# Kernel tuning notes

Measured on AMD Instinct MI355X. Metric: run time of the kernel, lower is better.

## Reference

```python
import jax, jax.numpy as jnp
import numpy as np

jax.config.update("jax_enable_x64", True)  # original casts to double for covpool/SVD

BN_EPS = 1e-5


def setup_inputs() -> dict:
    key = jax.random.key(0)
    k1, k2 = jax.random.split(key)
    x = jax.random.normal(k1, (64, 2048, 14, 14), dtype=jnp.float32)
    conv_w = jax.random.normal(k2, (256, 2048), dtype=jnp.float32) * 0.02  # 1x1 conv kernel
    bn_gamma = jnp.ones((256,), dtype=jnp.float32)
    bn_beta = jnp.zeros((256,), dtype=jnp.float32)
    return {"x": x, "conv_w": conv_w, "bn_gamma": bn_gamma, "bn_beta": bn_beta}


def reference(x, conv_w, bn_gamma, bn_beta):
    # --- dimension reduction block: 1x1 conv (no bias) + BN (train mode) + ReLU ---
    y = jnp.einsum('oc,bchw->bohw', conv_w, x)  # [B,256,14,14]
    mean = y.mean(axis=(0, 2, 3), keepdims=True)
    var = y.var(axis=(0, 2, 3), keepdims=True)
    y = (y - mean) * jax.lax.rsqrt(var + BN_EPS)
    y = y * bn_gamma[None, :, None, None] + bn_beta[None, :, None, None]
    y = jnp.maximum(y, 0.0)

    # --- Covpool: x @ (I/M - 11^T/M^2) @ x^T, in float64 as original ---
    B, d, h, w = y.shape
    M = h * w
    z = y.reshape(B, d, M).astype(jnp.float64)
    zc = z - z.mean(axis=2, keepdims=True)          # centering == multiplying by I_hat
    cov = jnp.einsum('bim,bjm->bij', zc, zc) / M    # [B,d,d], symmetric PSD

    # --- Eigen decomposition (SVD of symmetric PSD == eigh), clamp tiny eigvals ---
    s, V = jnp.linalg.eigh(cov)                     # s: [B,d], V: [B,d,d]
    eps = jnp.finfo(jnp.float64).eps
    s = jnp.maximum(s, eps)

    # --- Power: matrix square root Q = V sqrt(S) V^T ---
    Q = jnp.einsum('bij,bj,bkj->bik', V, jnp.sqrt(s), V)  # [B,d,d]

    # --- upper-triangular (incl. diag) vectorization, row-major like torch triu ---
    iu = jnp.triu_indices(d)
    q_triv = Q[:, iu[0], iu[1]]                     # [B, d*(d+1)/2]
    return q_triv.astype(jnp.float32)
```

## Files before the change

kernel.cpp:

```cpp
#include <hip/hip_runtime.h>
#include <hip/hip_bf16.h>

static constexpr int B   = 64;
static constexpr int CIN = 2048;
static constexpr int O   = 256;
static constexpr int HW  = 196;
static constexpr int D   = 256;
static constexpr int TRI = 32896;
static constexpr int NQ_COUPLED = 5;
static constexpr size_t NELEM = (size_t)B * D * D;
static constexpr size_t YN    = (size_t)B * O * HW;

typedef unsigned short u16;
typedef unsigned short u16x4 __attribute__((ext_vector_type(4)));
typedef unsigned short u16x8 __attribute__((ext_vector_type(8)));
typedef __bf16         bf16x8 __attribute__((ext_vector_type(8)));
typedef float          f32x4 __attribute__((ext_vector_type(4)));

static __device__ __forceinline__ u16 f2bf(float x) {
    unsigned int u = __float_as_uint(x);
    u += 0x7FFFu + ((u >> 16) & 1u);
    return (u16)(u >> 16);
}
static __device__ __forceinline__ float bf2f(u16 h) {
    return __uint_as_float(((unsigned int)h) << 16);
}
static __device__ __forceinline__ f32x4 mm_bf16(u16x8 a, u16x8 b, f32x4 c) {
    return __builtin_amdgcn_mfma_f32_16x16x32_bf16(
        __builtin_bit_cast(bf16x8, a), __builtin_bit_cast(bf16x8, b), c, 0, 0, 0);
}

__global__ __launch_bounds__(256) void k_wsplit(const float* __restrict__ W,
                                                u16* __restrict__ Wh,
                                                u16* __restrict__ Wl) {
    const size_t i = (size_t)blockIdx.x * 256 + threadIdx.x;
    const float v = W[i];
    const u16 h = f2bf(v);
    Wh[i] = h;
    Wl[i] = f2bf(v - bf2f(h));
}

__global__ __launch_bounds__(256, 3) void k_conv(const float* __restrict__ x,
                                                 const u16* __restrict__ Wh,
                                                 const u16* __restrict__ Wl,
                                                 float* __restrict__ psum) {
    const int l   = blockIdx.x;
    const int xcd = l & 7, u = l >> 3;
    const int q   = xcd * 98 + u;
    const int ks  = q & 3;
    const int t2  = q >> 2;
    const int ot  = t2 & 1, gt = t2 >> 1;
    const int o0  = ot * 128;
    const int cbase = ks * 512;
    float* yp = psum + (size_t)ks * YN;

    const int tid = threadIdx.x;

    __shared__ u16 sW[2][128][40], sX[2][128][40];

    const int colX  = tid & 127;
    const int chalf = (tid >> 7) * 16;
    const int gX = gt * 128 + colX;
    const int bX = gX / 196;
    const int mX = gX - bX * 196;
    const size_t xbase = (size_t)bX * (CIN * HW) + mX;

    const int rW = tid >> 1, kq = (tid & 1) * 16;
    const u16* gWh = Wh + (size_t)(o0 + rW) * CIN + cbase + kq;
    const u16* gWl = Wl + (size_t)(o0 + rW) * CIN + cbase + kq;

    const int lane = tid & 63, w = tid >> 6;
    const int wr = w >> 1, wc = w & 1;
    const int lr = lane & 15, lg = lane >> 4, ko = lg << 3;

    f32x4 acc[4][4] = {};

    u16x8 pWh[2], pWl[2];
    float pX[16];
    u16x4 cXh[4], cXl[4];

    auto loadW = [&](int kb) {
        #pragma unroll
        for (int qq = 0; qq < 2; ++qq) {
            pWh[qq] = *(const u16x8*)&gWh[kb + qq * 8];
            pWl[qq] = *(const u16x8*)&gWl[kb + qq * 8];
        }
    };
    auto loadX = [&](int kb) {
        #pragma unroll
        for (int i = 0; i < 16; ++i)
            pX[i] = x[xbase + (size_t)(cbase + kb + chalf + i) * HW];
    };
    auto convX = [&]() {
        #pragma unroll
        for (int i = 0; i < 16; i += 4) {
            u16x4 vh, vl;
            #pragma unroll
            for (int j = 0; j < 4; ++j) {
                const float v = pX[i + j];
                const u16 h = f2bf(v);
                vh[j] = h;
                vl[j] = f2bf(v - bf2f(h));
            }
            cXh[i >> 2] = vh;
            cXl[i >> 2] = vl;
        }
    };
    auto storeWX = [&]() {
        #pragma unroll
        for (int qq = 0; qq < 2; ++qq) {
            *(u16x8*)&sW[0][rW][kq + qq * 8] = pWh[qq];
            *(u16x8*)&sW[1][rW][kq + qq * 8] = pWl[qq];
        }
        #pragma unroll
        for (int qq = 0; qq < 4; ++qq) {
            *(u16x4*)&sX[0][colX][chalf + qq * 4] = cXh[qq];
            *(u16x4*)&sX[1][colX][chalf + qq * 4] = cXl[qq];
        }
    };
    auto compute = [&]() {
        u16x8 fah[4], fal[4], fbh[4], fbl[4];
        #pragma unroll
        for (int f = 0; f < 4; ++f) {
            fah[f] = *(const u16x8*)&sW[0][wr * 64 + f * 16 + lr][ko];
            fal[f] = *(const u16x8*)&sW[1][wr * 64 + f * 16 + lr][ko];
            fbh[f] = *(const u16x8*)&sX[0][wc * 64 + f * 16 + lr][ko];
            fbl[f] = *(const u16x8*)&sX[1][wc * 64 + f * 16 + lr][ko];
        }
        #pragma unroll
        for (int fi = 0; fi < 4; ++fi)
            #pragma unroll
            for (int fj = 0; fj < 4; ++fj) {
                acc[fi][fj] = mm_bf16(fah[fi], fbh[fj], acc[fi][fj]);
                acc[fi][fj] = mm_bf16(fah[fi], fbl[fj], acc[fi][fj]);
                acc[fi][fj] = mm_bf16(fal[fi], fbh[fj], acc[fi][fj]);
            }
    };

    loadW(0); loadX(0); convX();
    for (int st = 0; st < 16; ++st) {
        __syncthreads();
        storeWX();
        __syncthreads();
        if (st < 15) { loadW((st + 1) * 32); loadX((st + 1) * 32); }
        compute();
        if (st < 15) convX();
    }

    #pragma unroll
    for (int fj = 0; fj < 4; ++fj) {
        const int gcol = gt * 128 + wc * 64 + fj * 16 + lr;
        const int bb = gcol / 196;
        const int mm = gcol - bb * 196;
        const size_t ybase = (size_t)bb * (O * HW) + mm;
        #pragma unroll
        for (int fi = 0; fi < 4; ++fi)
            #pragma unroll
            for (int r = 0; r < 4; ++r) {
                const int orow = o0 + wr * 64 + fi * 16 + (lg << 2) + r;
                yp[ybase + (size_t)orow * HW] = acc[fi][fj][r];
            }
    }
}

__global__ __launch_bounds__(256) void k_redy(const float* __restrict__ ps,
                                              float* __restrict__ y) {
    const size_t i = ((size_t)blockIdx.x * 256 + threadIdx.x) * 4;
    if (i >= YN) return;
    float4 a = *(const float4*)&ps[i];
    const float4 b = *(const float4*)&ps[YN + i];
    const float4 c = *(const float4*)&ps[2 * YN + i];
    const float4 d = *(const float4*)&ps[3 * YN + i];
    a.x += b.x + c.x + d.x; a.y += b.y + c.y + d.y;
    a.z += b.z + c.z + d.z; a.w += b.w + c.w + d.w;
    *(float4*)&y[i] = a;
}

__global__ __launch_bounds__(256) void k_bnstats(const float* __restrict__ y,
                                                 const float* __restrict__ gamma,
                                                 const float* __restrict__ beta,
                                                 float* __restrict__ scl,
                                                 float* __restrict__ shf) {
    const int o = blockIdx.x;
    const int tid = threadIdx.x;
    float s = 0.f, s2 = 0.f;
    if (tid < HW) {
        for (int b = 0; b < B; ++b) {
            const float v = y[((size_t)b * O + o) * HW + tid];
            s += v; s2 += v * v;
        }
    }
    #pragma unroll
    for (int msk = 32; msk; msk >>= 1) {
        s  += __shfl_xor(s,  msk);
        s2 += __shfl_xor(s2, msk);
    }
    __shared__ float rs[4], rs2[4];
    if ((tid & 63) == 0) { rs[tid >> 6] = s; rs2[tid >> 6] = s2; }
    __syncthreads();
    if (tid == 0) {
        const float N = (float)(B * HW);
        const float ts  = rs[0] + rs[1] + rs[2] + rs[3];
        const float ts2 = rs2[0] + rs2[1] + rs2[2] + rs2[3];
        const float mean = ts / N;
        const float var  = ts2 / N - mean * mean;
        const float sc = gamma[o] * rsqrtf(var + 1e-5f);
        scl[o] = sc;
        shf[o] = beta[o] - mean * sc;
    }
}

__global__ __launch_bounds__(64) void k_center(float* __restrict__ z,
                                               const float* __restrict__ scl,
                                               const float* __restrict__ shf) {
    const int row = blockIdx.x;
    const int o = row & 255;
    const int lane = threadIdx.x;
    const float sc = scl[o], sh = shf[o];
    float* zr = &z[(size_t)row * HW];
    float vals[4];
    float s = 0.f;
    #pragma unroll
    for (int q = 0; q < 4; ++q) {
        const int m = q * 64 + lane;
        float v = 0.f;
        if (m < HW) v = fmaxf(fmaf(zr[m], sc, sh), 0.f);
        vals[q] = v; s += v;
    }
    #pragma unroll
    for (int msk = 32; msk; msk >>= 1) s += __shfl_xor(s, msk);
    const float mean = s / (float)HW;
    #pragma unroll
    for (int q = 0; q < 4; ++q) {
        const int m = q * 64 + lane;
        if (m < HW) zr[m] = vals[q] - mean;
    }
}

__global__ __launch_bounds__(256) void k_cov(const float* __restrict__ z,
                                             float* __restrict__ covf) {
    const int b = blockIdx.y;
    const int jt = blockIdx.x & 3, it = blockIdx.x >> 2;
    const int i0 = it * 64, j0 = jt * 64;
    const int tid = threadIdx.x;
    const int tn = tid & 15, tmq = tid >> 4;

    __shared__ float sA[28][68], sB[28][68];
    double acc[4][4] = {};
    const float* zb = &z[(size_t)b * D * HW];

    for (int k0 = 0; k0 < HW; k0 += 28) {
        #pragma unroll
        for (int q = 0; q < 7; ++q) {
            const int idx = tid + q * 256;
            const int r = idx / 28, kk = idx % 28;
            sA[kk][r] = zb[(size_t)(i0 + r) * HW + k0 + kk];
            sB[kk][r] = zb[(size_t)(j0 + r) * HW + k0 + kk];
        }
        __syncthreads();
        #pragma unroll
        for (int kk = 0; kk < 28; ++kk) {
            const float4 av = *reinterpret_cast<const float4*>(&sA[kk][tmq << 2]);
            const float4 bv = *reinterpret_cast<const float4*>(&sB[kk][tn << 2]);
            const double aa[4] = {av.x, av.y, av.z, av.w};
            const double bb[4] = {bv.x, bv.y, bv.z, bv.w};
            #pragma unroll
            for (int i = 0; i < 4; ++i)
                #pragma unroll
                for (int j = 0; j < 4; ++j)
                    acc[i][j] = fma(aa[i], bb[j], acc[i][j]);
        }
        __syncthreads();
    }
    const double inv = 1.0 / (double)HW;
    #pragma unroll
    for (int i = 0; i < 4; ++i)
        #pragma unroll
        for (int j = 0; j < 4; ++j)
            covf[(size_t)b * D * D + (size_t)(i0 + (tmq << 2) + i) * D
                 + j0 + (tn << 2) + j] = (float)(acc[i][j] * inv);
}

__global__ __launch_bounds__(256) void k_lmax(const float* __restrict__ covf,
                                              double* __restrict__ cn) {
    const int b = blockIdx.x;
    const int tid = threadIdx.x;
    const float* A = &covf[(size_t)b * 65536];
    __shared__ float vs[256];
    __shared__ float red[4];
    vs[tid] = 1.f;
    __syncthreads();
    float lam = 1.f;
    for (int it = 0; it < 6; ++it) {
        float u0 = 0.f, u1 = 0.f, u2 = 0.f, u3 = 0.f;
        #pragma unroll 8
        for (int k = 0; k < D; k += 4) {
            u0 = fmaf(A[(size_t)(k + 0) * D + tid], vs[k + 0], u0);
            u1 = fmaf(A[(size_t)(k + 1) * D + tid], vs[k + 1], u1);
            u2 = fmaf(A[(size_t)(k + 2) * D + tid], vs[k + 2], u2);
            u3 = fmaf(A[(size_t)(k + 3) * D + tid], vs[k + 3], u3);
        }
        const float uu = (u0 + u1) + (u2 + u3);
        float sq = uu * uu;
        #pragma unroll
        for (int msk = 32; msk; msk >>= 1) sq += __shfl_xor(sq, msk);
        __syncthreads();
        if ((tid & 63) == 0) red[tid >> 6] = sq;
        __syncthreads();
        const float nrm = sqrtf(red[0] + red[1] + red[2] + red[3]) + 1e-30f;
        lam = nrm;
        vs[tid] = uu / nrm;
        __syncthreads();
    }
    if (tid == 0) cn[b] = (lam > 1e-30f) ? 1.25 * (double)lam : 1.0;
}

__global__ __launch_bounds__(256) void k_init(const float* __restrict__ covf,
                                              const double* __restrict__ cn,
                                              u16* __restrict__ Yh,
                                              u16* __restrict__ Yl) {
    const size_t e = (size_t)blockIdx.x * 256 + threadIdx.x;
    const int b = (int)(e >> 16);
    const int ij = (int)(e & 65535);
    const float diag = ((ij >> 8) == (ij & 255)) ? 1e-7f : 0.f;
    const float f = covf[e] / (float)cn[b] + diag;
    const u16 h = f2bf(f);
    Yh[e] = h;
    Yl[e] = f2bf(f - bf2f(h));
}

template <int MODE, int FUSED>
__global__ __launch_bounds__(256, 2) void k_mgemm(
        const u16* __restrict__ A0h, const u16* __restrict__ A0l,
        const u16* __restrict__ B0h, const u16* __restrict__ B0l,
        u16* __restrict__ C0h, u16* __restrict__ C0l,
        const u16* __restrict__ A1h, const u16* __restrict__ A1l,
        const u16* __restrict__ B1h, const u16* __restrict__ B1l,
        u16* __restrict__ C1h, u16* __restrict__ C1l,
        const double* __restrict__ cn, float* __restrict__ outp) {
    const int orig = blockIdx.x;
    const int xcd  = orig & 7;
    const int s    = orig >> 3;
    int batch, task, opz;
    if (FUSED) {
        const int bl  = s / 12;
        const int rem = s - bl * 12;
        opz  = rem >= 6;
        task = rem - opz * 6;
        batch = xcd * 8 + bl;
    } else {
        opz = 0;
        const int bl = s / 6;
        task = s - bl * 6;
        batch = xcd * 8 + bl;
    }

    const u16 *Ah, *Al, *Bh, *Bl;
    u16 *Ch, *Cl;
    if (opz == 0) { Ah = A0h; Al = A0l; Bh = B0h; Bl = B0l; Ch = C0h; Cl = C0l; }
    else          { Ah = A1h; Al = A1l; Bh = B1h; Bl = B1l; Ch = C1h; Cl = C1l; }

    const int it = task >> 2;
    const int jt = (task < 4) ? task : task - 2;
    const int i0 = it * 128, j0 = jt * 64;
    const size_t boff = (size_t)batch * 65536;
    Ah += boff; Al += boff; Bh += boff; Bl += boff; Ch += boff; Cl += boff;

    const int tid = threadIdx.x;
    __shared__ u16 sA[2][128][72];
    __shared__ u16 sB[2][64][72];

    const int rA = tid >> 1, khA = (tid & 1) * 32;
    const u16* gAh = Ah + (size_t)(i0 + rA) * 256 + khA;
    const u16* gAl = Al + (size_t)(i0 + rA) * 256 + khA;
    const int rB = tid >> 2, khB = (tid & 3) * 16;
    const u16* gBh = Bh + (size_t)(j0 + rB) * 256 + khB;
    const u16* gBl = Bl + (size_t)(j0 + rB) * 256 + khB;

    const int lane = tid & 63, w = tid >> 6;
    const int wr = w >> 1, wc = w & 1;
    const int lr = lane & 15, lg = lane >> 4, ko = lg << 3;

    f32x4 acc[4][2] = {};

    u16x8 pAh[4], pAl[4], pBh[2], pBl[2];
    auto g_load = [&](int kb) {
        #pragma unroll
        for (int qq = 0; qq < 4; ++qq) {
            pAh[qq] = *(const u16x8*)&gAh[kb + qq * 8];
            pAl[qq] = *(const u16x8*)&gAl[kb + qq * 8];
        }
        #pragma unroll
        for (int qq = 0; qq < 2; ++qq) {
            pBh[qq] = *(const u16x8*)&gBh[kb + qq * 8];
            pBl[qq] = *(const u16x8*)&gBl[kb + qq * 8];
        }
    };
    auto s_store = [&]() {
        #pragma unroll
        for (int qq = 0; qq < 4; ++qq) {
            *(u16x8*)&sA[0][rA][khA + qq * 8] = pAh[qq];
            *(u16x8*)&sA[1][rA][khA + qq * 8] = pAl[qq];
        }
        #pragma unroll
        for (int qq = 0; qq < 2; ++qq) {
            *(u16x8*)&sB[0][rB][khB + qq * 8] = pBh[qq];
            *(u16x8*)&sB[1][rB][khB + qq * 8] = pBl[qq];
        }
    };
    auto compute = [&]() {
        #pragma unroll
        for (int kr = 0; kr < 2; ++kr) {
            const int kk = kr * 32 + ko;
            u16x8 fah[4], fal[4], fbh[2], fbl[2];
            #pragma unroll
            for (int f = 0; f < 4; ++f) {
                fah[f] = *(const u16x8*)&sA[0][wr * 64 + f * 16 + lr][kk];
                fal[f] = *(const u16x8*)&sA[1][wr * 64 + f * 16 + lr][kk];
            }
            #pragma unroll
            for (int f = 0; f < 2; ++f) {
                fbh[f] = *(const u16x8*)&sB[0][wc * 32 + f * 16 + lr][kk];
                fbl[f] = *(const u16x8*)&sB[1][wc * 32 + f * 16 + lr][kk];
            }
            #pragma unroll
            for (int fi = 0; fi < 4; ++fi)
                #pragma unroll
                for (int fj = 0; fj < 2; ++fj) {
                    acc[fi][fj] = mm_bf16(fah[fi], fbh[fj], acc[fi][fj]);
                    acc[fi][fj] = mm_bf16(fah[fi], fbl[fj], acc[fi][fj]);
                    acc[fi][fj] = mm_bf16(fal[fi], fbh[fj], acc[fi][fj]);
                }
        }
    };

    g_load(0);
    for (int st = 0; st < 4; ++st) {
        __syncthreads();
        s_store();
        __syncthreads();
        if (st < 3) g_load((st + 1) * 64);
        compute();
    }

    const int orow = wr * 64 + (lg << 2);
    const int ocol = wc * 32 + lr;

    if (MODE == 3) {
        const double sc = sqrt(cn[batch]);
        #pragma unroll
        for (int fi = 0; fi < 4; ++fi)
            #pragma unroll
            for (int r = 0; r < 4; ++r) {
                const int gi = i0 + orow + fi * 16 + r;
                const size_t rowoff = (size_t)gi * D - ((size_t)gi * (gi - 1)) / 2;
                #pragma unroll
                for (int fj = 0; fj < 2; ++fj) {
                    const int gj = j0 + ocol + fj * 16;
                    if (gj >= gi)
                        outp[(size_t)batch * TRI + rowoff + (gj - gi)] =
                            (float)(sc * (double)acc[fi][fj][r]);
                }
            }
        return;
    }

    u16 hv[4][4][2], lv[4][4][2];
    #pragma unroll
    for (int fi = 0; fi < 4; ++fi)
        #pragma unroll
        for (int r = 0; r < 4; ++r) {
            const int gi = i0 + orow + fi * 16 + r;
            #pragma unroll
            for (int fj = 0; fj < 2; ++fj) {
                const int gj = j0 + ocol + fj * 16;
                float v = acc[fi][fj][r];
                if (MODE == 1) {
                    const size_t xo = (size_t)gi * 256 + gj;
                    const float xv = bf2f(Ah[xo]) + bf2f(Al[xo]);
                    v = (((gi == gj) ? 15.0f : 0.0f) - 10.0f * xv + 3.0f * v) * 0.125f;
                }
                const u16 h = f2bf(v);
                const u16 lo = f2bf(v - bf2f(h));
                const size_t co = (size_t)gi * 256 + gj;
                Ch[co] = h;
                Cl[co] = lo;
                hv[fi][r][fj] = h;
                lv[fi][r][fj] = lo;
            }
        }

    if (task == 2 || task == 3) {
        __syncthreads();
        u16 (*tH)[136] = reinterpret_cast<u16(*)[136]>(&sA[0][0][0]);
        u16 (*tL)[136] = reinterpret_cast<u16(*)[136]>(&sB[0][0][0]);
        #pragma unroll
        for (int fi = 0; fi < 4; ++fi)
            #pragma unroll
            for (int r = 0; r < 4; ++r) {
                const int li = orow + fi * 16 + r;
                #pragma unroll
                for (int fj = 0; fj < 2; ++fj) {
                    const int lj = ocol + fj * 16;
                    tH[lj][li] = hv[fi][r][fj];
                    tL[lj][li] = lv[fi][r][fj];
                }
            }
        __syncthreads();
        const int r2 = tid >> 2, c2 = (tid & 3) << 5;
        const size_t mo = (size_t)(j0 + r2) * 256 + i0 + c2;
        #pragma unroll
        for (int qq = 0; qq < 4; ++qq) {
            *(u16x8*)&Ch[mo + qq * 8] = *(const u16x8*)&tH[r2][c2 + qq * 8];
            *(u16x8*)&Cl[mo + qq * 8] = *(const u16x8*)&tL[r2][c2 + qq * 8];
        }
    }
}

extern "C" void kernel_launch(void* const* d_in, const int* in_sizes, int n_in,
                              void* d_out, int out_size, void* d_ws, size_t ws_size,
                              hipStream_t stream) {
    const float* x     = (const float*)d_in[0];
    const float* W     = (const float*)d_in[1];
    const float* gamma = (const float*)d_in[2];
    const float* beta  = (const float*)d_in[3];
    float* out = (float*)d_out;

    char* ws = (char*)d_ws;
    size_t off = 0;
    auto alloc = [&](size_t bytes) -> void* {
        void* p = ws + off;
        off += (bytes + 255) & ~(size_t)255;
        return p;
    };
    float*  y    = (float*)alloc(YN * sizeof(float));
    float*  covf = (float*)alloc(NELEM * sizeof(float));
    float*  scl  = (float*)alloc(O * sizeof(float));
    float*  shf  = (float*)alloc(O * sizeof(float));
    double* cn   = (double*)alloc(B * sizeof(double));
    u16*    Wh   = (u16*)alloc((size_t)O * CIN * sizeof(u16));
    u16*    Wl   = (u16*)alloc((size_t)O * CIN * sizeof(u16));
    u16* pl = (u16*)alloc(12 * NELEM * sizeof(u16));
    if (off > ws_size) return;
    u16 *YAh = pl,             *YAl = pl + NELEM;
    u16 *YBh = pl + 2 * NELEM, *YBl = pl + 3 * NELEM;
    u16 *MAh = pl + 4 * NELEM, *MAl = pl + 5 * NELEM;
    u16 *MBh = pl + 6 * NELEM, *MBl = pl + 7 * NELEM;
    u16 *Rh  = pl + 8 * NELEM, *Rl  = pl + 9 * NELEM;
    u16 *Uh  = pl + 10 * NELEM,*Ul  = pl + 11 * NELEM;
    float* psum = (float*)pl;

    k_wsplit <<<(O * CIN) / 256, 256, 0, stream>>>(W, Wh, Wl);
    k_conv   <<<784, 256, 0, stream>>>(x, Wh, Wl, psum);
    k_redy   <<<3136, 256, 0, stream>>>(psum, y);
    k_bnstats<<<O, 256, 0, stream>>>(y, gamma, beta, scl, shf);
    k_center <<<B * O, 64, 0, stream>>>(y, scl, shf);
    k_cov    <<<dim3(16, B), 256, 0, stream>>>(y, covf);
    k_lmax   <<<B, 256, 0, stream>>>(covf, cn);
    k_init   <<<B * 256, 256, 0, stream>>>(covf, cn, YAh, YAl);

    k_mgemm<1, 0><<<384, 256, 0, stream>>>(YAh, YAl, YAh, YAl, Rh, Rl,
                                           YAh, YAl, YAh, YAl, Rh, Rl, cn, out);
    k_mgemm<2, 0><<<384, 256, 0, stream>>>(YAh, YAl, Rh, Rl, YBh, YBl,
                                           YAh, YAl, Rh, Rl, YBh, YBl, cn, out);
    k_mgemm<2, 0><<<384, 256, 0, stream>>>(Rh, Rl, YBh, YBl, MBh, MBl,
                                           Rh, Rl, YBh, YBl, MBh, MBl, cn, out);

    u16 *Ych = YBh, *Ycl = YBl, *Yah = YAh, *Yal = YAl;
    u16 *Mch = MBh, *Mcl = MBl, *Mah = MAh, *Mal = MAl;
    for (int itq = 0; itq < NQ_COUPLED; ++itq) {
        k_mgemm<1, 0><<<384, 256, 0, stream>>>(Mch, Mcl, Mch, Mcl, Rh, Rl,
                                               Mch, Mcl, Mch, Mcl, Rh, Rl, cn, out);
        k_mgemm<2, 1><<<768, 256, 0, stream>>>(Ych, Ycl, Rh, Rl, Yah, Yal,
                                               Mch, Mcl, Rh, Rl, Uh, Ul, cn, out);
        k_mgemm<2, 0><<<384, 256, 0, stream>>>(Rh, Rl, Uh, Ul, Mah, Mal,
                                               Rh, Rl, Uh, Ul, Mah, Mal, cn, out);
        u16* t;
        t = Ych; Ych = Yah; Yah = t;  t = Ycl; Ycl = Yal; Yal = t;
        t = Mch; Mch = Mah; Mah = t;  t = Mcl; Mcl = Mal; Mal = t;
    }
    k_mgemm<1, 0><<<384, 256, 0, stream>>>(Mch, Mcl, Mch, Mcl, Rh, Rl,
                                           Mch, Mcl, Mch, Mcl, Rh, Rl, cn, out);
    k_mgemm<3, 0><<<384, 256, 0, stream>>>(Ych, Ycl, Rh, Rl, Uh, Ul,
                                           Ych, Ycl, Rh, Rl, Uh, Ul, cn, out);
}
```

Baseline: 508.3 us.

## Compute full matrix tiles with smaller k-step and fuse partial-sum reduction into BN stats

The matrix-iteration GEMM stops exploiting symmetry: it now computes all 8 output tiles per batch instead of 6 plus a transpose write. It shrinks the shared-memory k-step from 64 to 32 so that 3 blocks fit per CU, and stages the epilogue through LDS for coalesced vector stores and vectorized loads of the residual operand. Separately, the split-K partial-sum reduction kernel is folded into the BN statistics kernel, removing one launch and one pass over y. This adds a third more MFMA work per GEMM in exchange for higher occupancy, uniform tiles and coalesced epilogues.

Measured after the change: 576.1 us. 1.13x slower.

```diff
diff --git a/kernel.cpp b/kernel.cpp
--- a/kernel.cpp
+++ b/kernel.cpp
@@ -163,20 +163,8 @@
     }
 }
 
-__global__ __launch_bounds__(256) void k_redy(const float* __restrict__ ps,
-                                              float* __restrict__ y) {
-    const size_t i = ((size_t)blockIdx.x * 256 + threadIdx.x) * 4;
-    if (i >= YN) return;
-    float4 a = *(const float4*)&ps[i];
-    const float4 b = *(const float4*)&ps[YN + i];
-    const float4 c = *(const float4*)&ps[2 * YN + i];
-    const float4 d = *(const float4*)&ps[3 * YN + i];
-    a.x += b.x + c.x + d.x; a.y += b.y + c.y + d.y;
-    a.z += b.z + c.z + d.z; a.w += b.w + c.w + d.w;
-    *(float4*)&y[i] = a;
-}
-
-__global__ __launch_bounds__(256) void k_bnstats(const float* __restrict__ y,
+__global__ __launch_bounds__(256) void k_bnstats(const float* __restrict__ ps,
+                                                 float* __restrict__ y,
                                                  const float* __restrict__ gamma,
                                                  const float* __restrict__ beta,
                                                  float* __restrict__ scl,
@@ -186,7 +174,10 @@
     float s = 0.f, s2 = 0.f;
     if (tid < HW) {
         for (int b = 0; b < B; ++b) {
-            const float v = y[((size_t)b * O + o) * HW + tid];
+            const size_t idx = ((size_t)b * O + o) * HW + tid;
+            const float v = ps[idx] + ps[YN + idx] + ps[2 * YN + idx]
+                          + ps[3 * YN + idx];
+            y[idx] = v;
             s += v; s2 += v * v;
         }
     }
@@ -330,7 +321,7 @@
 }
 
 template <int MODE, int FUSED>
-__global__ __launch_bounds__(256, 2) void k_mgemm(
+__global__ __launch_bounds__(256, 3) void k_mgemm(
         const u16* __restrict__ A0h, const u16* __restrict__ A0l,
         const u16* __restrict__ B0h, const u16* __restrict__ B0l,
         u16* __restrict__ C0h, u16* __restrict__ C0l,
@@ -341,18 +332,17 @@
     const int orig = blockIdx.x;
     const int xcd  = orig & 7;
     const int s    = orig >> 3;
-    int batch, task, opz;
+    int batch, tile, opz;
     if (FUSED) {
-        const int bl  = s / 12;
-        const int rem = s - bl * 12;
-        opz  = rem >= 6;
-        task = rem - opz * 6;
+        const int bl  = s >> 4;
+        const int opq = s & 15;
+        opz  = opq >> 3;
+        tile = opq & 7;
         batch = xcd * 8 + bl;
     } else {
         opz = 0;
-        const int bl = s / 6;
-        task = s - bl * 6;
-        batch = xcd * 8 + bl;
+        batch = xcd * 8 + (s >> 3);
+        tile = s & 7;
     }
 
     const u16 *Ah, *Al, *Bh, *Bl;
@@ -360,20 +350,23 @@
     if (opz == 0) { Ah = A0h; Al = A0l; Bh = B0h; Bl = B0l; Ch = C0h; Cl = C0l; }
     else          { Ah = A1h; Al = A1l; Bh = B1h; Bl = B1l; Ch = C1h; Cl = C1l; }
 
-    const int it = task >> 2;
-    const int jt = (task < 4) ? task : task - 2;
-    const int i0 = it * 128, j0 = jt * 64;
+    const int i0 = (tile >> 2) * 128, j0 = (tile & 3) * 64;
     const size_t boff = (size_t)batch * 65536;
     Ah += boff; Al += boff; Bh += boff; Bl += boff; Ch += boff; Cl += boff;
 
     const int tid = threadIdx.x;
-    __shared__ u16 sA[2][128][72];
-    __shared__ u16 sB[2][64][72];
-
-    const int rA = tid >> 1, khA = (tid & 1) * 32;
+    __shared__ u16 smem[18432];
+    u16* sA0 = smem;
+    u16* sA1 = smem + 5120;
+    u16* sB0 = smem + 10240;
+    u16* sB1 = smem + 12800;
+    u16* ep0 = smem;
+    u16* ep1 = smem + 9216;
+
+    const int rA = tid >> 1, khA = (tid & 1) * 16;
     const u16* gAh = Ah + (size_t)(i0 + rA) * 256 + khA;
     const u16* gAl = Al + (size_t)(i0 + rA) * 256 + khA;
-    const int rB = tid >> 2, khB = (tid & 3) * 16;
+    const int rB = tid >> 2, khB = (tid & 3) * 8;
     const u16* gBh = Bh + (size_t)(j0 + rB) * 256 + khB;
     const u16* gBl = Bl + (size_t)(j0 + rB) * 256 + khB;
 
@@ -383,63 +376,51 @@
 
     f32x4 acc[4][2] = {};
 
-    u16x8 pAh[4], pAl[4], pBh[2], pBl[2];
+    u16x8 pAh[2], pAl[2], pBh, pBl;
     auto g_load = [&](int kb) {
-        #pragma unroll
-        for (int qq = 0; qq < 4; ++qq) {
-            pAh[qq] = *(const u16x8*)&gAh[kb + qq * 8];
-            pAl[qq] = *(const u16x8*)&gAl[kb + qq * 8];
-        }
-        #pragma unroll
-        for (int qq = 0; qq < 2; ++qq) {
-            pBh[qq] = *(const u16x8*)&gBh[kb + qq * 8];
-            pBl[qq] = *(const u16x8*)&gBl[kb + qq * 8];
-        }
+        pAh[0] = *(const u16x8*)&gAh[kb];
+        pAh[1] = *(const u16x8*)&gAh[kb + 8];
+        pAl[0] = *(const u16x8*)&gAl[kb];
+        pAl[1] = *(const u16x8*)&gAl[kb + 8];
+        pBh = *(const u16x8*)&gBh[kb];
+        pBl = *(const u16x8*)&gBl[kb];
     };
     auto s_store = [&]() {
-        #pragma unroll
-        for (int qq = 0; qq < 4; ++qq) {
-            *(u16x8*)&sA[0][rA][khA + qq * 8] = pAh[qq];
-            *(u16x8*)&sA[1][rA][khA + qq * 8] = pAl[qq];
-        }
-        #pragma unroll
-        for (int qq = 0; qq < 2; ++qq) {
-            *(u16x8*)&sB[0][rB][khB + qq * 8] = pBh[qq];
-            *(u16x8*)&sB[1][rB][khB + qq * 8] = pBl[qq];
-        }
+        *(u16x8*)&sA0[rA * 40 + khA]     = pAh[0];
+        *(u16x8*)&sA0[rA * 40 + khA + 8] = pAh[1];
+        *(u16x8*)&sA1[rA * 40 + khA]     = pAl[0];
+        *(u16x8*)&sA1[rA * 40 + khA + 8] = pAl[1];
+        *(u16x8*)&sB0[rB * 40 + khB]     = pBh;
+        *(u16x8*)&sB1[rB * 40 + khB]     = pBl;
     };
     auto compute = [&]() {
-        #pragma unroll
-        for (int kr = 0; kr < 2; ++kr) {
-            const int kk = kr * 32 + ko;
-            u16x8 fah[4], fal[4], fbh[2], fbl[2];
-            #pragma unroll
-            for (int f = 0; f < 4; ++f) {
-                fah[f] = *(const u16x8*)&sA[0][wr * 64 + f * 16 + lr][kk];
-                fal[f] = *(const u16x8*)&sA[1][wr * 64 + f * 16 + lr][kk];
+        u16x8 fah[4], fal[4], fbh[2], fbl[2];
+        #pragma unroll
+        for (int f = 0; f < 4; ++f) {
+            fah[f] = *(const u16x8*)&sA0[(wr * 64 + f * 16 + lr) * 40 + ko];
+            fal[f] = *(const u16x8*)&sA1[(wr * 64 + f * 16 + lr) * 40 + ko];
+        }
+        #pragma unroll
+        for (int f = 0; f < 2; ++f) {
+            fbh[f] = *(const u16x8*)&sB0[(wc * 32 + f * 16 + lr) * 40 + ko];
+            fbl[f] = *(const u16x8*)&sB1[(wc * 32 + f * 16 + lr) * 40 + ko];
+        }
+        #pragma unroll
+        for (int fi = 0; fi < 4; ++fi)
+            #pragma unroll
+            for (int fj = 0; fj < 2; ++fj) {
+                acc[fi][fj] = mm_bf16(fah[fi], fbh[fj], acc[fi][fj]);
+                acc[fi][fj] = mm_bf16(fah[fi], fbl[fj], acc[fi][fj]);
+                acc[fi][fj] = mm_bf16(fal[fi], fbh[fj], acc[fi][fj]);
             }
-            #pragma unroll
-            for (int f = 0; f < 2; ++f) {
-                fbh[f] = *(const u16x8*)&sB[0][wc * 32 + f * 16 + lr][kk];
-                fbl[f] = *(const u16x8*)&sB[1][wc * 32 + f * 16 + lr][kk];
-            }
-            #pragma unroll
-            for (int fi = 0; fi < 4; ++fi)
-                #pragma unroll
-                for (int fj = 0; fj < 2; ++fj) {
-                    acc[fi][fj] = mm_bf16(fah[fi], fbh[fj], acc[fi][fj]);
-                    acc[fi][fj] = mm_bf16(fah[fi], fbl[fj], acc[fi][fj]);
-                    acc[fi][fj] = mm_bf16(fal[fi], fbh[fj], acc[fi][fj]);
-                }
-        }
     };
 
     g_load(0);
-    for (int st = 0; st < 4; ++st) {
+    for (int st = 0; st < 8; ++st) {
         __syncthreads();
         s_store();
         __syncthreads();
-        if (st < 3) g_load((st + 1) * 64);
+        if (st < 7) g_load((st + 1) * 32);
         compute();
     }
 
@@ -465,55 +446,49 @@
         return;
     }
 
-    u16 hv[4][4][2], lv[4][4][2];
+    __syncthreads();
+    const int er = tid >> 1, ec = (tid & 1) * 32;
+    if (MODE == 1) {
+        u16x8 th[4], tl[4];
+        #pragma unroll
+        for (int qq = 0; qq < 4; ++qq) {
+            th[qq] = *(const u16x8*)&Ah[(size_t)(i0 + er) * 256 + j0 + ec + qq * 8];
+            tl[qq] = *(const u16x8*)&Al[(size_t)(i0 + er) * 256 + j0 + ec + qq * 8];
+        }
+        #pragma unroll
+        for (int qq = 0; qq < 4; ++qq) {
+            *(u16x8*)&ep0[er * 72 + ec + qq * 8] = th[qq];
+            *(u16x8*)&ep1[er * 72 + ec + qq * 8] = tl[qq];
+        }
+        __syncthreads();
+    }
     #pragma unroll
     for (int fi = 0; fi < 4; ++fi)
         #pragma unroll
         for (int r = 0; r < 4; ++r) {
-            const int gi = i0 + orow + fi * 16 + r;
+            const int li = orow + fi * 16 + r;
             #pragma unroll
             for (int fj = 0; fj < 2; ++fj) {
-                const int gj = j0 + ocol + fj * 16;
+                const int lj = ocol + fj * 16;
                 float v = acc[fi][fj][r];
                 if (MODE == 1) {
-                    const size_t xo = (size_t)gi * 256 + gj;
-                    const float xv = bf2f(Ah[xo]) + bf2f(Al[xo]);
-                    v = (((gi == gj) ? 15.0f : 0.0f) - 10.0f * xv + 3.0f * v) * 0.125f;
+                    const float xv = bf2f(ep0[li * 72 + lj]) + bf2f(ep1[li * 72 + lj]);
+                    v = ((((i0 + li) == (j0 + lj)) ? 15.0f : 0.0f)
+                         - 10.0f * xv + 3.0f * v) * 0.125f;
                 }
                 const u16 h = f2bf(v);
                 const u16 lo = f2bf(v - bf2f(h));
-                const size_t co = (size_t)gi * 256 + gj;
-                Ch[co] = h;
-                Cl[co] = lo;
-                hv[fi][r][fj] = h;
-                lv[fi][r][fj] = lo;
+                ep0[li * 72 + lj] = h;
+                ep1[li * 72 + lj] = lo;
             }
         }
-
-    if (task == 2 || task == 3) {
-        __syncthreads();
-        u16 (*tH)[136] = reinterpret_cast<u16(*)[136]>(&sA[0][0][0]);
-        u16 (*tL)[136] = reinterpret_cast<u16(*)[136]>(&sB[0][0][0]);
-        #pragma unroll
-        for (int fi = 0; fi < 4; ++fi)
-            #pragma unroll
-            for (int r = 0; r < 4; ++r) {
-                const int li = orow + fi * 16 + r;
-                #pragma unroll
-                for (int fj = 0; fj < 2; ++fj) {
-                    const int lj = ocol + fj * 16;
-                    tH[lj][li] = hv[fi][r][fj];
-                    tL[lj][li] = lv[fi][r][fj];
-                }
-            }
-        __syncthreads();
-        const int r2 = tid >> 2, c2 = (tid & 3) << 5;
-        const size_t mo = (size_t)(j0 + r2) * 256 + i0 + c2;
-        #pragma unroll
-        for (int qq = 0; qq < 4; ++qq) {
-            *(u16x8*)&Ch[mo + qq * 8] = *(const u16x8*)&tH[r2][c2 + qq * 8];
-            *(u16x8*)&Cl[mo + qq * 8] = *(const u16x8*)&tL[r2][c2 + qq * 8];
-        }
+    __syncthreads();
+    #pragma unroll
+    for (int qq = 0; qq < 4; ++qq) {
+        *(u16x8*)&Ch[(size_t)(i0 + er) * 256 + j0 + ec + qq * 8] =
+            *(const u16x8*)&ep0[er * 72 + ec + qq * 8];
+        *(u16x8*)&Cl[(size_t)(i0 + er) * 256 + j0 + ec + qq * 8] =
+            *(const u16x8*)&ep1[er * 72 + ec + qq * 8];
     }
 }
 
@@ -552,35 +527,34 @@
 
     k_wsplit <<<(O * CIN) / 256, 256, 0, stream>>>(W, Wh, Wl);
     k_conv   <<<784, 256, 0, stream>>>(x, Wh, Wl, psum);
-    k_redy   <<<3136, 256, 0, stream>>>(psum, y);
-    k_bnstats<<<O, 256, 0, stream>>>(y, gamma, beta, scl, shf);
+    k_bnstats<<<O, 256, 0, stream>>>(psum, y, gamma, beta, scl, shf);
     k_center <<<B * O, 64, 0, stream>>>(y, scl, shf);
     k_cov    <<<dim3(16, B), 256, 0, stream>>>(y, covf);
     k_lmax   <<<B, 256, 0, stream>>>(covf, cn);
     k_init   <<<B * 256, 256, 0, stream>>>(covf, cn, YAh, YAl);
 
-    k_mgemm<1, 0><<<384, 256, 0, stream>>>(YAh, YAl, YAh, YAl, Rh, Rl,
+    k_mgemm<1, 0><<<512, 256, 0, stream>>>(YAh, YAl, YAh, YAl, Rh, Rl,
                                            YAh, YAl, YAh, YAl, Rh, Rl, cn, out);
-    k_mgemm<2, 0><<<384, 256, 0, stream>>>(YAh, YAl, Rh, Rl, YBh, YBl,
+    k_mgemm<2, 0><<<512, 256, 0, stream>>>(YAh, YAl, Rh, Rl, YBh, YBl,
                                            YAh, YAl, Rh, Rl, YBh, YBl, cn, out);
-    k_mgemm<2, 0><<<384, 256, 0, stream>>>(Rh, Rl, YBh, YBl, MBh, MBl,
+    k_mgemm<2, 0><<<512, 256, 0, stream>>>(Rh, Rl, YBh, YBl, MBh, MBl,
                                            Rh, Rl, YBh, YBl, MBh, MBl, cn, out);
 
     u16 *Ych = YBh, *Ycl = YBl, *Yah = YAh, *Yal = YAl;
     u16 *Mch = MBh, *Mcl = MBl, *Mah = MAh, *Mal = MAl;
     for (int itq = 0; itq < NQ_COUPLED; ++itq) {
-        k_mgemm<1, 0><<<384, 256, 0, stream>>>(Mch, Mcl, Mch, Mcl, Rh, Rl,
+        k_mgemm<1, 0><<<512, 256, 0, stream>>>(Mch, Mcl, Mch, Mcl, Rh, Rl,
                                                Mch, Mcl, Mch, Mcl, Rh, Rl, cn, out);
-        k_mgemm<2, 1><<<768, 256, 0, stream>>>(Ych, Ycl, Rh, Rl, Yah, Yal,
-                                               Mch, Mcl, Rh, Rl, Uh, Ul, cn, out);
-        k_mgemm<2, 0><<<384, 256, 0, stream>>>(Rh, Rl, Uh, Ul, Mah, Mal,
+        k_mgemm<2, 1><<<1024, 256, 0, stream>>>(Ych, Ycl, Rh, Rl, Yah, Yal,
+                                                Mch, Mcl, Rh, Rl, Uh, Ul, cn, out);
+        k_mgemm<2, 0><<<512, 256, 0, stream>>>(Rh, Rl, Uh, Ul, Mah, Mal,
                                                Rh, Rl, Uh, Ul, Mah, Mal, cn, out);
         u16* t;
         t = Ych; Ych = Yah; Yah = t;  t = Ycl; Ycl = Yal; Yal = t;
         t = Mch; Mch = Mah; Mah = t;  t = Mcl; Mcl = Mal; Mal = t;
     }
-    k_mgemm<1, 0><<<384, 256, 0, stream>>>(Mch, Mcl, Mch, Mcl, Rh, Rl,
+    k_mgemm<1, 0><<<512, 256, 0, stream>>>(Mch, Mcl, Mch, Mcl, Rh, Rl,
                                            Mch, Mcl, Mch, Mcl, Rh, Rl, cn, out);
-    k_mgemm<3, 0><<<384, 256, 0, stream>>>(Ych, Ycl, Rh, Rl, Uh, Ul,
+    k_mgemm<3, 0><<<512, 256, 0, stream>>>(Ych, Ycl, Rh, Rl, Uh, Ul,
                                            Ych, Ycl, Rh, Rl, Uh, Ul, cn, out);
 }
```

## Use full 128x128 tiles in matrix GEMMs, dropping symmetric transpose-mirroring

Applied to the files above, without the earlier changes.

Each GEMM block now computes a 128x128 output tile, with four quadrants per batch, instead of 128x64 tiles that covered only the upper triangle. The lower triangle was previously filled by an LDS transpose and mirror store; that path is removed and all four quadrants are computed directly. The final triu-output pass launches only the three quadrants that contain upper-triangle entries. This raises per-block MFMA work and register use (acc grows to 4x4) and cuts launched blocks from 384 to 256. It also spends about a third more matrix FLOPs in exchange for removing the transpose epilogue and its extra synchronisation.

Result: no change. 518.1 us (+1.9%).

```diff
diff --git a/kernel.cpp b/kernel.cpp
--- a/kernel.cpp
+++ b/kernel.cpp
@@ -341,18 +341,23 @@
     const int orig = blockIdx.x;
     const int xcd  = orig & 7;
     const int s    = orig >> 3;
-    int batch, task, opz;
+    int batch, quad, opz;
     if (FUSED) {
-        const int bl  = s / 12;
-        const int rem = s - bl * 12;
-        opz  = rem >= 6;
-        task = rem - opz * 6;
+        const int bl  = s >> 3;
+        const int opq = s & 7;
+        opz  = opq >> 2;
+        quad = opq & 3;
         batch = xcd * 8 + bl;
+    } else if (MODE == 3) {
+        opz = 0;
+        const int bl = s / 3;
+        const int m3 = s - bl * 3;
+        batch = xcd * 8 + bl;
+        quad = (m3 == 0) ? 0 : ((m3 == 1) ? 1 : 3);
     } else {
         opz = 0;
-        const int bl = s / 6;
-        task = s - bl * 6;
-        batch = xcd * 8 + bl;
+        batch = xcd * 8 + (s >> 2);
+        quad = s & 3;
     }
 
     const u16 *Ah, *Al, *Bh, *Bl;
@@ -360,38 +365,31 @@
     if (opz == 0) { Ah = A0h; Al = A0l; Bh = B0h; Bl = B0l; Ch = C0h; Cl = C0l; }
     else          { Ah = A1h; Al = A1l; Bh = B1h; Bl = B1l; Ch = C1h; Cl = C1l; }
 
-    const int it = task >> 2;
-    const int jt = (task < 4) ? task : task - 2;
-    const int i0 = it * 128, j0 = jt * 64;
+    const int i0 = (quad >> 1) * 128, j0 = (quad & 1) * 128;
     const size_t boff = (size_t)batch * 65536;
     Ah += boff; Al += boff; Bh += boff; Bl += boff; Ch += boff; Cl += boff;
 
     const int tid = threadIdx.x;
-    __shared__ u16 sA[2][128][72];
-    __shared__ u16 sB[2][64][72];
-
-    const int rA = tid >> 1, khA = (tid & 1) * 32;
-    const u16* gAh = Ah + (size_t)(i0 + rA) * 256 + khA;
-    const u16* gAl = Al + (size_t)(i0 + rA) * 256 + khA;
-    const int rB = tid >> 2, khB = (tid & 3) * 16;
-    const u16* gBh = Bh + (size_t)(j0 + rB) * 256 + khB;
-    const u16* gBl = Bl + (size_t)(j0 + rB) * 256 + khB;
+    __shared__ u16 sA[2][128][72], sB[2][128][72];
+
+    const int rW = tid >> 1, kh = (tid & 1) * 32;
+    const u16* gAh = Ah + (size_t)(i0 + rW) * 256 + kh;
+    const u16* gAl = Al + (size_t)(i0 + rW) * 256 + kh;
+    const u16* gBh = Bh + (size_t)(j0 + rW) * 256 + kh;
+    const u16* gBl = Bl + (size_t)(j0 + rW) * 256 + kh;
 
     const int lane = tid & 63, w = tid >> 6;
     const int wr = w >> 1, wc = w & 1;
     const int lr = lane & 15, lg = lane >> 4, ko = lg << 3;
 
-    f32x4 acc[4][2] = {};
-
-    u16x8 pAh[4], pAl[4], pBh[2], pBl[2];
+    f32x4 acc[4][4] = {};
+
+    u16x8 pAh[4], pAl[4], pBh[4], pBl[4];
     auto g_load = [&](int kb) {
         #pragma unroll
         for (int qq = 0; qq < 4; ++qq) {
             pAh[qq] = *(const u16x8*)&gAh[kb + qq * 8];
             pAl[qq] = *(const u16x8*)&gAl[kb + qq * 8];
-        }
-        #pragma unroll
-        for (int qq = 0; qq < 2; ++qq) {
             pBh[qq] = *(const u16x8*)&gBh[kb + qq * 8];
             pBl[qq] = *(const u16x8*)&gBl[kb + qq * 8];
         }
@@ -399,34 +397,28 @@
     auto s_store = [&]() {
         #pragma unroll
         for (int qq = 0; qq < 4; ++qq) {
-            *(u16x8*)&sA[0][rA][khA + qq * 8] = pAh[qq];
-            *(u16x8*)&sA[1][rA][khA + qq * 8] = pAl[qq];
-        }
-        #pragma unroll
-        for (int qq = 0; qq < 2; ++qq) {
-            *(u16x8*)&sB[0][rB][khB + qq * 8] = pBh[qq];
-            *(u16x8*)&sB[1][rB][khB + qq * 8] = pBl[qq];
+            *(u16x8*)&sA[0][rW][kh + qq * 8] = pAh[qq];
+            *(u16x8*)&sA[1][rW][kh + qq * 8] = pAl[qq];
+            *(u16x8*)&sB[0][rW][kh + qq * 8] = pBh[qq];
+            *(u16x8*)&sB[1][rW][kh + qq * 8] = pBl[qq];
         }
     };
     auto compute = [&]() {
         #pragma unroll
         for (int kr = 0; kr < 2; ++kr) {
             const int kk = kr * 32 + ko;
-            u16x8 fah[4], fal[4], fbh[2], fbl[2];
+            u16x8 fah[4], fal[4], fbh[4], fbl[4];
             #pragma unroll
             for (int f = 0; f < 4; ++f) {
                 fah[f] = *(const u16x8*)&sA[0][wr * 64 + f * 16 + lr][kk];
                 fal[f] = *(const u16x8*)&sA[1][wr * 64 + f * 16 + lr][kk];
-            }
-            #pragma unroll
-            for (int f = 0; f < 2; ++f) {
-                fbh[f] = *(const u16x8*)&sB[0][wc * 32 + f * 16 + lr][kk];
-                fbl[f] = *(const u16x8*)&sB[1][wc * 32 + f * 16 + lr][kk];
+                fbh[f] = *(const u16x8*)&sB[0][wc * 64 + f * 16 + lr][kk];
+                fbl[f] = *(const u16x8*)&sB[1][wc * 64 + f * 16 + lr][kk];
             }
             #pragma unroll
             for (int fi = 0; fi < 4; ++fi)
                 #pragma unroll
-                for (int fj = 0; fj < 2; ++fj) {
+                for (int fj = 0; fj < 4; ++fj) {
                     acc[fi][fj] = mm_bf16(fah[fi], fbh[fj], acc[fi][fj]);
                     acc[fi][fj] = mm_bf16(fah[fi], fbl[fj], acc[fi][fj]);
                     acc[fi][fj] = mm_bf16(fal[fi], fbh[fj], acc[fi][fj]);
@@ -444,7 +436,7 @@
     }
 
     const int orow = wr * 64 + (lg << 2);
-    const int ocol = wc * 32 + lr;
+    const int ocol = wc * 64 + lr;
 
     if (MODE == 3) {
         const double sc = sqrt(cn[batch]);
@@ -455,7 +447,7 @@
                 const int gi = i0 + orow + fi * 16 + r;
                 const size_t rowoff = (size_t)gi * D - ((size_t)gi * (gi - 1)) / 2;
                 #pragma unroll
-                for (int fj = 0; fj < 2; ++fj) {
+                for (int fj = 0; fj < 4; ++fj) {
                     const int gj = j0 + ocol + fj * 16;
                     if (gj >= gi)
                         outp[(size_t)batch * TRI + rowoff + (gj - gi)] =
@@ -465,14 +457,13 @@
         return;
     }
 
-    u16 hv[4][4][2], lv[4][4][2];
     #pragma unroll
     for (int fi = 0; fi < 4; ++fi)
         #pragma unroll
         for (int r = 0; r < 4; ++r) {
             const int gi = i0 + orow + fi * 16 + r;
             #pragma unroll
-            for (int fj = 0; fj < 2; ++fj) {
+            for (int fj = 0; fj < 4; ++fj) {
                 const int gj = j0 + ocol + fj * 16;
                 float v = acc[fi][fj][r];
                 if (MODE == 1) {
@@ -485,36 +476,8 @@
                 const size_t co = (size_t)gi * 256 + gj;
                 Ch[co] = h;
                 Cl[co] = lo;
-                hv[fi][r][fj] = h;
-                lv[fi][r][fj] = lo;
             }
         }
-
-    if (task == 2 || task == 3) {
-        __syncthreads();
-        u16 (*tH)[136] = reinterpret_cast<u16(*)[136]>(&sA[0][0][0]);
-        u16 (*tL)[136] = reinterpret_cast<u16(*)[136]>(&sB[0][0][0]);
-        #pragma unroll
-        for (int fi = 0; fi < 4; ++fi)
-            #pragma unroll
-            for (int r = 0; r < 4; ++r) {
-                const int li = orow + fi * 16 + r;
-                #pragma unroll
-                for (int fj = 0; fj < 2; ++fj) {
-                    const int lj = ocol + fj * 16;
-                    tH[lj][li] = hv[fi][r][fj];
-                    tL[lj][li] = lv[fi][r][fj];
-                }
-            }
-        __syncthreads();
-        const int r2 = tid >> 2, c2 = (tid & 3) << 5;
-        const size_t mo = (size_t)(j0 + r2) * 256 + i0 + c2;
-        #pragma unroll
-        for (int qq = 0; qq < 4; ++qq) {
-            *(u16x8*)&Ch[mo + qq * 8] = *(const u16x8*)&tH[r2][c2 + qq * 8];
-            *(u16x8*)&Cl[mo + qq * 8] = *(const u16x8*)&tL[r2][c2 + qq * 8];
-        }
-    }
 }
 
 extern "C" void kernel_launch(void* const* d_in, const int* in_sizes, int n_in,
@@ -559,28 +522,28 @@
     k_lmax   <<<B, 256, 0, stream>>>(covf, cn);
     k_init   <<<B * 256, 256, 0, stream>>>(covf, cn, YAh, YAl);
 
-    k_mgemm<1, 0><<<384, 256, 0, stream>>>(YAh, YAl, YAh, YAl, Rh, Rl,
+    k_mgemm<1, 0><<<256, 256, 0, stream>>>(YAh, YAl, YAh, YAl, Rh, Rl,
                                            YAh, YAl, YAh, YAl, Rh, Rl, cn, out);
-    k_mgemm<2, 0><<<384, 256, 0, stream>>>(YAh, YAl, Rh, Rl, YBh, YBl,
+    k_mgemm<2, 0><<<256, 256, 0, stream>>>(YAh, YAl, Rh, Rl, YBh, YBl,
                                            YAh, YAl, Rh, Rl, YBh, YBl, cn, out);
-    k_mgemm<2, 0><<<384, 256, 0, stream>>>(Rh, Rl, YBh, YBl, MBh, MBl,
+    k_mgemm<2, 0><<<256, 256, 0, stream>>>(Rh, Rl, YBh, YBl, MBh, MBl,
                                            Rh, Rl, YBh, YBl, MBh, MBl, cn, out);
 
     u16 *Ych = YBh, *Ycl = YBl, *Yah = YAh, *Yal = YAl;
     u16 *Mch = MBh, *Mcl = MBl, *Mah = MAh, *Mal = MAl;
     for (int itq = 0; itq < NQ_COUPLED; ++itq) {
-        k_mgemm<1, 0><<<384, 256, 0, stream>>>(Mch, Mcl, Mch, Mcl, Rh, Rl,
+        k_mgemm<1, 0><<<256, 256, 0, stream>>>(Mch, Mcl, Mch, Mcl, Rh, Rl,
                                                Mch, Mcl, Mch, Mcl, Rh, Rl, cn, out);
-        k_mgemm<2, 1><<<768, 256, 0, stream>>>(Ych, Ycl, Rh, Rl, Yah, Yal,
+        k_mgemm<2, 1><<<512, 256, 0, stream>>>(Ych, Ycl, Rh, Rl, Yah, Yal,
                                                Mch, Mcl, Rh, Rl, Uh, Ul, cn, out);
-        k_mgemm<2, 0><<<384, 256, 0, stream>>>(Rh, Rl, Uh, Ul, Mah, Mal,
+        k_mgemm<2, 0><<<256, 256, 0, stream>>>(Rh, Rl, Uh, Ul, Mah, Mal,
                                                Rh, Rl, Uh, Ul, Mah, Mal, cn, out);
         u16* t;
         t = Ych; Ych = Yah; Yah = t;  t = Ycl; Ycl = Yal; Yal = t;
         t = Mch; Mch = Mah; Mah = t;  t = Mcl; Mcl = Mal; Mal = t;
     }
-    k_mgemm<1, 0><<<384, 256, 0, stream>>>(Mch, Mcl, Mch, Mcl, Rh, Rl,
+    k_mgemm<1, 0><<<256, 256, 0, stream>>>(Mch, Mcl, Mch, Mcl, Rh, Rl,
                                            Mch, Mcl, Mch, Mcl, Rh, Rl, cn, out);
-    k_mgemm<3, 0><<<384, 256, 0, stream>>>(Ych, Ycl, Rh, Rl, Uh, Ul,
+    k_mgemm<3, 0><<<192, 256, 0, stream>>>(Ych, Ycl, Rh, Rl, Uh, Ul,
                                            Ych, Ycl, Rh, Rl, Uh, Ul, cn, out);
 }
```
